# Optimization experiments

Measured on AMD Instinct MI355X. Metric: run time of the kernel, lower is better.

Reference implementation:

```python
import jax, jax.numpy as jnp
import numpy as np

N = 50000      # nodes
E = 1600000    # edges (before self loops)
B = 512        # graphs
D = 128        # gcn dim (constant across the 3 GAT layers)
H = 1024       # hidden_dim
O = 128        # output_dim
NEG_SLOPE = 0.2


def setup_inputs() -> dict:
    key = jax.random.key(0)
    ks = jax.random.split(key, 24)
    inp = {
        "x": jax.random.normal(ks[0], (N, D), jnp.float32),
        "edge_index": jax.random.randint(ks[1], (2, E), 0, N, dtype=jnp.int64),
        "edge_weight": jax.random.uniform(ks[2], (E,), jnp.float32),
        "batch": jnp.sort(jax.random.randint(ks[3], (N,), 0, B, dtype=jnp.int64)),
    }
    s = 1.0 / np.sqrt(D)
    for i in range(3):
        k = 4 + 4 * i
        inp[f"W{i+1}"] = jax.random.normal(ks[k], (D, D), jnp.float32) * s
        inp[f"as{i+1}"] = jax.random.normal(ks[k + 1], (D,), jnp.float32) * s
        inp[f"ad{i+1}"] = jax.random.normal(ks[k + 2], (D,), jnp.float32) * s
        inp[f"b{i+1}"] = jnp.zeros((D,), jnp.float32)
    inp["Wf1"] = jax.random.normal(ks[16], (D, H), jnp.float32) * s
    inp["bf1"] = jnp.zeros((H,), jnp.float32)
    inp["Wf2"] = jax.random.normal(ks[17], (H, O), jnp.float32) * (1.0 / np.sqrt(H))
    inp["bf2"] = jnp.zeros((O,), jnp.float32)
    return inp


def gat_conv(x, src, dst, W, a_src, a_dst, b):
    """PyG GATConv, heads=1: gather -> leakyrelu -> segment softmax -> scatter-add."""
    h = x @ W                                   # [N, D]
    e = jax.nn.leaky_relu(jnp.take(h @ a_src, src) + jnp.take(h @ a_dst, dst), NEG_SLOPE)  # [E']
    m = jax.ops.segment_max(e, dst, num_segments=N)
    ex = jnp.exp(e - m[dst])
    denom = jax.ops.segment_sum(ex, dst, num_segments=N)
    alpha = ex / denom[dst]                      # segment softmax over incoming edges
    out = jax.ops.segment_sum(alpha[:, None] * h[src], dst, num_segments=N)
    return out + b


def reference(x, edge_index, edge_weight, batch,
              W1, as1, ad1, b1, W2, as2, ad2, b2, W3, as3, ad3, b3,
              Wf1, bf1, Wf2, bf2):
    # GATConv adds self loops; edge_weight is unused by GATConv (faithful to original)
    loop = jnp.arange(N, dtype=edge_index.dtype)
    src = jnp.concatenate([edge_index[0], loop])
    dst = jnp.concatenate([edge_index[1], loop])

    h = gat_conv(x, src, dst, W1, as1, ad1, b1)
    h = jax.nn.relu(gat_conv(h, src, dst, W2, as2, ad2, b2))
    h = jax.nn.relu(gat_conv(h, src, dst, W3, as3, ad3, b3))

    # global mean pool (gep)
    sums = jax.ops.segment_sum(h, batch, num_segments=B)        # [B, D]
    counts = jax.ops.segment_sum(jnp.ones((N,), h.dtype), batch, num_segments=B)
    pooled = sums / jnp.maximum(counts, 1.0)[:, None]

    # MLP head; dropout is identity at inference
    o = jax.nn.relu(pooled) @ Wf1 + bf1
    o = jax.nn.relu(o) @ Wf2 + bf2
    return o
```

## Files before the change

### kernel.cpp

```cpp
#include <hip/hip_runtime.h>
#include <cstdint>
#include <cstddef>

#define NEG_SLOPE 0.2f

typedef _Float16 f16x8 __attribute__((ext_vector_type(8)));
typedef float f32x4v __attribute__((ext_vector_type(4)));

__device__ __forceinline__ unsigned enc_f(float f) {
  unsigned u = __float_as_uint(f);
  return (u & 0x80000000u) ? ~u : (u | 0x80000000u);
}
__device__ __forceinline__ float dec_f(unsigned u) {
  return (u & 0x80000000u) ? __uint_as_float(u ^ 0x80000000u) : __uint_as_float(~u);
}

#define AST 136
#define ABYTES (64 * AST * 2)
#define SMEM_BYTES (ABYTES + 4 * 64 * 2 * 4)

__global__ void k_bounds_prep(const int* __restrict__ batch, int N, int B,
                              int* __restrict__ gstart, unsigned* __restrict__ maxPart,
                              int* __restrict__ counts,
                              const float* __restrict__ W1, const float* __restrict__ W2,
                              const float* __restrict__ W3,
                              const float* __restrict__ Wf1, const float* __restrict__ Wf2,
                              _Float16* __restrict__ Wt1, _Float16* __restrict__ Wt2,
                              _Float16* __restrict__ Wt3,
                              _Float16* __restrict__ Wf1t, _Float16* __restrict__ Wf2t,
                              int nbb) {
  int b = blockIdx.x;
  if (b >= nbb) {
    int ti = b - nbb;
    const float* src;
    _Float16* dst;
    int lds_, ldd_, k0, n0;
    if (ti < 3) {
      src = (ti == 0) ? W1 : (ti == 1) ? W2 : W3;
      dst = (ti == 0) ? Wt1 : (ti == 1) ? Wt2 : Wt3;
      lds_ = 128; ldd_ = 128; k0 = 0; n0 = 0;
    } else if (ti < 11) {
      int j = ti - 3;
      src = Wf1; dst = Wf1t; lds_ = 1024; ldd_ = 128; k0 = 0; n0 = j * 128;
    } else {
      int j = ti - 11;
      src = Wf2; dst = Wf2t; lds_ = 128; ldd_ = 1024; k0 = j * 128; n0 = 0;
    }
    for (int i = threadIdx.x; i < 2048; i += 256) {
      int k = i >> 4, n8 = (i & 15) << 3;
      const float* s = &src[(size_t)(k0 + k) * lds_ + n0 + n8];
      float4 v0 = *(const float4*)&s[0];
      float4 v1 = *(const float4*)&s[4];
      dst[(size_t)(n0 + n8 + 0) * ldd_ + k0 + k] = (_Float16)v0.x;
      dst[(size_t)(n0 + n8 + 1) * ldd_ + k0 + k] = (_Float16)v0.y;
      dst[(size_t)(n0 + n8 + 2) * ldd_ + k0 + k] = (_Float16)v0.z;
      dst[(size_t)(n0 + n8 + 3) * ldd_ + k0 + k] = (_Float16)v0.w;
      dst[(size_t)(n0 + n8 + 4) * ldd_ + k0 + k] = (_Float16)v1.x;
      dst[(size_t)(n0 + n8 + 5) * ldd_ + k0 + k] = (_Float16)v1.y;
      dst[(size_t)(n0 + n8 + 6) * ldd_ + k0 + k] = (_Float16)v1.z;
      dst[(size_t)(n0 + n8 + 7) * ldd_ + k0 + k] = (_Float16)v1.w;
    }
    return;
  }
  int n = b * blockDim.x + threadIdx.x;
  if (n < 768) maxPart[n] = 0u;
  if (n >= N) return;
  counts[n] = 0;
  int cur = batch[n];
  if (n == 0) {
    for (int g = 0; g <= cur; g++) gstart[g] = 0;
  } else {
    int prev = batch[n - 1];
    for (int g = prev + 1; g <= cur; g++) gstart[g] = n;
  }
  if (n == N - 1) {
    for (int g = cur + 1; g <= B; g++) gstart[g] = N;
  }
}

__global__ void k_count_rank(const int* __restrict__ dst, int E,
                             int* counts, int* __restrict__ rank) {
  int e = blockIdx.x * blockDim.x + threadIdx.x;
  if (e < E) rank[e] = atomicAdd(&counts[dst[e]], 1);
}

__global__ __launch_bounds__(1024) void k_scan1(const int* __restrict__ counts, int N,
                                                int* __restrict__ row_ptr, int* __restrict__ part) {
  __shared__ int tmp[1024];
  int t = threadIdx.x;
  int i = blockIdx.x * 1024 + t;
  int v = (i < N) ? 1 + counts[i] : 0;
  tmp[t] = v;
  __syncthreads();
  for (int off = 1; off < 1024; off <<= 1) {
    int u = (t >= off) ? tmp[t - off] : 0;
    __syncthreads();
    tmp[t] += u;
    __syncthreads();
  }
  if (i < N) row_ptr[i + 1] = tmp[t];
  if (t == 1023) part[blockIdx.x] = tmp[t];
}

__global__ __launch_bounds__(1024) void k_scan3(int* __restrict__ row_ptr,
                                                const int* __restrict__ part, int N) {
  __shared__ int s_off;
  int bi = blockIdx.x;
  if (threadIdx.x == 0) {
    int run = 0;
    for (int b = 0; b < bi; b++) run += part[b];
    s_off = run;
    if (bi == 0) row_ptr[0] = 0;
  }
  __syncthreads();
  int i = bi * 1024 + threadIdx.x;
  if (i < N) row_ptr[i + 1] += s_off;
}

__device__ __forceinline__ void gemm_body(char* smem, int bx,
                                          const float* __restrict__ A32,
                                          const unsigned short* __restrict__ A16,
                                          const _Float16* __restrict__ WtG,
                                          unsigned short* __restrict__ hb,
                                          const float* __restrict__ asrc,
                                          const float* __restrict__ adst,
                                          float* __restrict__ sv, float* __restrict__ dv,
                                          unsigned* __restrict__ maxSlot, int M) {
  _Float16* Ah = (_Float16*)smem;
  float (*sred)[64][2] = (float (*)[64][2])(smem + ABYTES);
  int t = threadIdx.x;
  int rowbase = bx * 64;

  if (A16) {
    for (int i = t; i < 64 * 16; i += 256) {
      int r = i >> 4, c8 = (i & 15) << 3;
      int gr = rowbase + r;
      uint4 v = make_uint4(0u, 0u, 0u, 0u);
      if (gr < M) v = *(const uint4*)&A16[(size_t)gr * 128 + c8];
      *(uint4*)&Ah[r * AST + c8] = v;
    }
  } else {
    for (int i = t; i < 64 * 32; i += 256) {
      int r = i >> 5, c4 = (i & 31) << 2;
      int gr = rowbase + r;
      float4 v = make_float4(0.f, 0.f, 0.f, 0.f);
      if (gr < M) v = *(const float4*)&A32[(size_t)gr * 128 + c4];
      _Float16 tmp[4] = {(_Float16)v.x, (_Float16)v.y, (_Float16)v.z, (_Float16)v.w};
      *(short4*)&Ah[r * AST + c4] = *(short4*)tmp;
    }
  }
  __syncthreads();

  int wave = t >> 6, lane = t & 63, quad = lane >> 4, l15 = lane & 15;
  f32x4v acc[4][2];
#pragma unroll
  for (int mt = 0; mt < 4; mt++)
#pragma unroll
    for (int nt = 0; nt < 2; nt++) {
      acc[mt][nt][0] = 0.f; acc[mt][nt][1] = 0.f; acc[mt][nt][2] = 0.f; acc[mt][nt][3] = 0.f;
    }

#pragma unroll
  for (int s = 0; s < 4; s++) {
    int k0 = (s << 5) + (quad << 3);
    f16x8 af[4], bf[2];
#pragma unroll
    for (int mt = 0; mt < 4; mt++)
      af[mt] = *(f16x8*)&Ah[(mt * 16 + l15) * AST + k0];
#pragma unroll
    for (int nt = 0; nt < 2; nt++)
      bf[nt] = *(const f16x8*)&WtG[(size_t)(wave * 32 + nt * 16 + l15) * 128 + k0];
#pragma unroll
    for (int mt = 0; mt < 4; mt++)
#pragma unroll
      for (int nt = 0; nt < 2; nt++)
        acc[mt][nt] = __builtin_amdgcn_mfma_f32_16x16x32_f16(af[mt], bf[nt], acc[mt][nt], 0, 0, 0);
  }
  __syncthreads();

  float avv0 = asrc[wave * 32 + l15],      avv1 = asrc[wave * 32 + 16 + l15];
  float adv0 = adst[wave * 32 + l15],      adv1 = adst[wave * 32 + 16 + l15];
  _Float16* hS16 = (_Float16*)smem;
#pragma unroll
  for (int mt = 0; mt < 4; mt++) {
#pragma unroll
    for (int rr = 0; rr < 4; rr++) {
      int row = mt * 16 + quad * 4 + rr;
      hS16[row * AST + wave * 32 + l15]      = (_Float16)acc[mt][0][rr];
      hS16[row * AST + wave * 32 + 16 + l15] = (_Float16)acc[mt][1][rr];
      float ps = acc[mt][0][rr] * avv0 + acc[mt][1][rr] * avv1;
      float pd = acc[mt][0][rr] * adv0 + acc[mt][1][rr] * adv1;
#pragma unroll
      for (int mask = 8; mask; mask >>= 1) {
        ps += __shfl_xor(ps, mask);
        pd += __shfl_xor(pd, mask);
      }
      if (l15 == 0) { sred[wave][row][0] = ps; sred[wave][row][1] = pd; }
    }
  }
  __syncthreads();

  int tx = t & 31, ty = t >> 5;
#pragma unroll
  for (int r8 = 0; r8 < 8; r8++) {
    int row = r8 * 8 + ty;
    int gr = rowbase + row;
    if (gr < M)
      *(uint2*)&hb[(size_t)gr * 128 + tx * 4] = *(const uint2*)&hS16[row * AST + tx * 4];
  }

  if (t < 64) {
    int gr = rowbase + t;
    float ps = sred[0][t][0] + sred[1][t][0] + sred[2][t][0] + sred[3][t][0];
    float pd = sred[0][t][1] + sred[1][t][1] + sred[2][t][1] + sred[3][t][1];
    float wmax = -1e30f;
    if (gr < M) { sv[gr] = ps; dv[gr] = pd; wmax = ps; }
#pragma unroll
    for (int mask = 32; mask; mask >>= 1) wmax = fmaxf(wmax, __shfl_xor(wmax, mask));
    if (t == 0) atomicMax(&maxSlot[bx & 255], enc_f(wmax));
  }
}

__global__ __launch_bounds__(256) void k_fill_gemm(const int* __restrict__ src,
                                                   const int* __restrict__ dst,
                                                   const int* __restrict__ rank, int E, int N,
                                                   const int* __restrict__ row_ptr,
                                                   int* __restrict__ col,
                                                   const float* __restrict__ A32,
                                                   const _Float16* __restrict__ WtG,
                                                   unsigned short* __restrict__ hb,
                                                   const float* __restrict__ asrc,
                                                   const float* __restrict__ adst,
                                                   float* __restrict__ sv, float* __restrict__ dv,
                                                   unsigned* __restrict__ maxSlot, int Gg) {
  __shared__ __align__(16) char smem[SMEM_BYTES];
  int b = (int)blockIdx.x;
  bool isGemm = ((b % 9) == 4) && ((b / 9) < Gg);
  if (isGemm) {
    gemm_body(smem, b / 9, A32, (const unsigned short*)nullptr, WtG,
              hb, asrc, adst, sv, dv, maxSlot, N);
  } else {
    int nGemmBefore = (b >= 4) ? min((b - 4) / 9 + 1, Gg) : 0;
    int i = (b - nGemmBefore) * 256 + threadIdx.x;
    if (i < N) col[row_ptr[i]] = i;
    int e = i - N;
    if (e >= 0 && e < E) col[row_ptr[dst[e]] + 1 + rank[e]] = src[e];
  }
}

__global__ __launch_bounds__(256) void k_gemm_fused(const unsigned short* __restrict__ A16,
                                                    const _Float16* __restrict__ WtG,
                                                    unsigned short* __restrict__ hb,
                                                    const float* __restrict__ asrc,
                                                    const float* __restrict__ adst,
                                                    float* __restrict__ sv, float* __restrict__ dv,
                                                    unsigned* __restrict__ maxSlot, int M) {
  __shared__ __align__(16) char smem[SMEM_BYTES];
  gemm_body(smem, (int)blockIdx.x, (const float*)nullptr, A16, WtG,
            hb, asrc, adst, sv, dv, maxSlot, M);
}

__global__ __launch_bounds__(256) void k_agg(const unsigned short* __restrict__ hb,
                                             const float* __restrict__ sv,
                                             const float* __restrict__ dv,
                                             const int* __restrict__ row_ptr,
                                             const int* __restrict__ col,
                                             const float* __restrict__ bias,
                                             const unsigned* __restrict__ maxSlot,
                                             unsigned short* __restrict__ out16,
                                             int N, int relu) {
  int wid = (int)((blockIdx.x * (size_t)blockDim.x + threadIdx.x) >> 6);
  int lane = threadIdx.x & 63;
  if (wid >= N) return;

  unsigned mp = max(max(maxSlot[lane], maxSlot[lane + 64]),
                    max(maxSlot[lane + 128], maxSlot[lane + 192]));
#pragma unroll
  for (int off = 32; off; off >>= 1) mp = max(mp, __shfl_xor(mp, off));
  float maxS = dec_f(mp);

  int beg = row_ptr[wid], end = row_ptr[wid + 1];
  float dn = dv[wid];
  float m = maxS + dn;
  m = (m > 0.f) ? m : NEG_SLOPE * m;

  int g = lane >> 4, sub = lane & 15;
  const uint32_t* hbu = (const uint32_t*)hb;
  float acc[8];
#pragma unroll
  for (int k = 0; k < 8; k++) acc[k] = 0.f;
  float dsum = 0.f;

#define FETCH_SLOT(K, W, H)                                                \
  {                                                                        \
    int sl = ((K) << 2) + g;                                               \
    int sn = __shfl(sn_l, sl);                                             \
    W = __shfl(w_l, sl);                                                   \
    H = make_uint4(0u, 0u, 0u, 0u);                                        \
    if (sl < cnt) H = *(const uint4*)(hbu + (size_t)sn * 64 + sub * 4);    \
  }
#define ACC_SLOT(W, H)                                                     \
  {                                                                        \
    const _Float16* hp = (const _Float16*)&H;                              \
    _Pragma("unroll")                                                      \
    for (int q = 0; q < 8; q++) acc[q] += W * (float)hp[q];                \
  }

  for (int base = beg; base < end; base += 64) {
    int cnt = min(end - base, 64);

    int sn_l = 0;
    float w_l = 0.f;
    if (lane < cnt) {
      sn_l = col[base + lane];
      float e = sv[sn_l] + dn;
      e = (e > 0.f) ? e : NEG_SLOPE * e;
      w_l = __expf(e - m);
      dsum += w_l;
    }

    int kmaxW4 = (((cnt + 3) >> 2) + 3) & ~3;
    float wA, wB, wC, wD;
    uint4 hA, hB, hC, hD;
    FETCH_SLOT(0, wA, hA);
    FETCH_SLOT(1, wB, hB);
    FETCH_SLOT(2, wC, hC);
    FETCH_SLOT(3, wD, hD);
    for (int k = 4; k < kmaxW4; k += 4) {
      ACC_SLOT(wA, hA); FETCH_SLOT(k + 0, wA, hA);
      ACC_SLOT(wB, hB); FETCH_SLOT(k + 1, wB, hB);
      ACC_SLOT(wC, hC); FETCH_SLOT(k + 2, wC, hC);
      ACC_SLOT(wD, hD); FETCH_SLOT(k + 3, wD, hD);
    }
    ACC_SLOT(wA, hA);
    ACC_SLOT(wB, hB);
    ACC_SLOT(wC, hC);
    ACC_SLOT(wD, hD);
  }

#pragma unroll
  for (int off = 1; off < 64; off <<= 1) dsum += __shfl_xor(dsum, off);
#pragma unroll
  for (int k = 0; k < 8; k++) {
    acc[k] += __shfl_xor(acc[k], 16);
    acc[k] += __shfl_xor(acc[k], 32);
  }
  if (lane < 16) {
    float inv = 1.f / dsum;
    float o[8];
    const float* bp = &bias[sub * 8];
#pragma unroll
    for (int k = 0; k < 8; k++) {
      o[k] = acc[k] * inv + bp[k];
      if (relu) o[k] = fmaxf(o[k], 0.f);
    }
    _Float16 q[8];
#pragma unroll
    for (int k = 0; k < 8; k++) q[k] = (_Float16)o[k];
    *(uint4*)&out16[(size_t)wid * 128 + sub * 8] = *(uint4*)q;
  }
}

__global__ __launch_bounds__(256) void k_pool(const unsigned short* __restrict__ h16,
                                              const int* __restrict__ gstart,
                                              unsigned short* __restrict__ pooled16, int B) {
  __shared__ float red[4][128];
  int b = blockIdx.x, t = threadIdx.x;
  int c = t & 63, seg = t >> 6;
  int s0 = gstart[b], s1 = gstart[b + 1];
  int cnt = s1 - s0;
  int per = (cnt + 3) >> 2;
  int n0 = s0 + seg * per;
  int n1 = min(n0 + per, s1);
  const uint32_t* hu = (const uint32_t*)h16;
  float a0 = 0.f, a1 = 0.f;
  for (int n = n0; n < n1; n++) {
    union { uint32_t u; _Float16 h[2]; } cv;
    cv.u = hu[(size_t)n * 64 + c];
    a0 += (float)cv.h[0];
    a1 += (float)cv.h[1];
  }
  if (seg) { red[seg][2 * c] = a0; red[seg][2 * c + 1] = a1; }
  __syncthreads();
  if (seg == 0) {
    a0 += red[1][2 * c] + red[2][2 * c] + red[3][2 * c];
    a1 += red[1][2 * c + 1] + red[2][2 * c + 1] + red[3][2 * c + 1];
    float inv = 1.f / (float)(cnt > 0 ? cnt : 1);
    union { uint32_t u; _Float16 h[2]; } ov;
    ov.h[0] = (_Float16)fmaxf(a0 * inv, 0.f);
    ov.h[1] = (_Float16)fmaxf(a1 * inv, 0.f);
    *(uint32_t*)&pooled16[(size_t)b * 128 + 2 * c] = ov.u;
  }
}

__global__ __launch_bounds__(256) void k_mlp1(const unsigned short* __restrict__ P16,
                                              const _Float16* __restrict__ Wf1t,
                                              const float* __restrict__ bf1,
                                              unsigned short* __restrict__ H1g, int B, int nRow) {
  __shared__ __align__(16) _Float16 Ah[64 * AST];
  int bx = (int)blockIdx.x;
  int rowt = bx % nRow, colt = bx / nRow;
  int rowbase = rowt * 64;
  int t = threadIdx.x;

  for (int i = t; i < 64 * 16; i += 256) {
    int r = i >> 4, c8 = (i & 15) << 3;
    int gr = rowbase + r;
    uint4 v = make_uint4(0u, 0u, 0u, 0u);
    if (gr < B) v = *(const uint4*)&P16[(size_t)gr * 128 + c8];
    *(uint4*)&Ah[r * AST + c8] = v;
  }
  __syncthreads();

  int wave = t >> 6, lane = t & 63, quad = lane >> 4, l15 = lane & 15;
  int colbase = colt * 128 + wave * 32;
  f32x4v acc[4][2];
#pragma unroll
  for (int mt = 0; mt < 4; mt++)
#pragma unroll
    for (int nt = 0; nt < 2; nt++) {
      acc[mt][nt][0] = 0.f; acc[mt][nt][1] = 0.f; acc[mt][nt][2] = 0.f; acc[mt][nt][3] = 0.f;
    }
#pragma unroll
  for (int s = 0; s < 4; s++) {
    int k0 = (s << 5) + (quad << 3);
    f16x8 af[4], bf[2];
#pragma unroll
    for (int mt = 0; mt < 4; mt++)
      af[mt] = *(f16x8*)&Ah[(mt * 16 + l15) * AST + k0];
#pragma unroll
    for (int nt = 0; nt < 2; nt++)
      bf[nt] = *(const f16x8*)&Wf1t[(size_t)(colbase + nt * 16 + l15) * 128 + k0];
#pragma unroll
    for (int mt = 0; mt < 4; mt++)
#pragma unroll
      for (int nt = 0; nt < 2; nt++)
        acc[mt][nt] = __builtin_amdgcn_mfma_f32_16x16x32_f16(af[mt], bf[nt], acc[mt][nt], 0, 0, 0);
  }

  float b0 = bf1[colbase + l15], b1 = bf1[colbase + 16 + l15];
#pragma unroll
  for (int mt = 0; mt < 4; mt++)
#pragma unroll
    for (int rr = 0; rr < 4; rr++) {
      int gr = rowbase + mt * 16 + quad * 4 + rr;
      if (gr < B) {
        H1g[(size_t)gr * 1024 + colbase + l15] =
            (unsigned short)__builtin_bit_cast(unsigned short, (_Float16)fmaxf(acc[mt][0][rr] + b0, 0.f));
        H1g[(size_t)gr * 1024 + colbase + 16 + l15] =
            (unsigned short)__builtin_bit_cast(unsigned short, (_Float16)fmaxf(acc[mt][1][rr] + b1, 0.f));
      }
    }
}

__global__ __launch_bounds__(256) void k_mlp2(const unsigned short* __restrict__ H1g,
                                              const _Float16* __restrict__ Wf2t,
                                              const float* __restrict__ bf2,
                                              float* __restrict__ out, int B) {
  __shared__ __align__(16) _Float16 Ah[64 * AST];
  int rowbase = (int)blockIdx.x * 64;
  int t = threadIdx.x;
  int wave = t >> 6, lane = t & 63, quad = lane >> 4, l15 = lane & 15;

  f32x4v acc[4][2];
#pragma unroll
  for (int mt = 0; mt < 4; mt++)
#pragma unroll
    for (int nt = 0; nt < 2; nt++) {
      acc[mt][nt][0] = 0.f; acc[mt][nt][1] = 0.f; acc[mt][nt][2] = 0.f; acc[mt][nt][3] = 0.f;
    }

  for (int kc = 0; kc < 8; kc++) {
    for (int i = t; i < 64 * 16; i += 256) {
      int r = i >> 4, c8 = (i & 15) << 3;
      int gr = rowbase + r;
      uint4 v = make_uint4(0u, 0u, 0u, 0u);
      if (gr < B) v = *(const uint4*)&H1g[(size_t)gr * 1024 + kc * 128 + c8];
      *(uint4*)&Ah[r * AST + c8] = v;
    }
    __syncthreads();
#pragma unroll
    for (int s = 0; s < 4; s++) {
      int k0 = (s << 5) + (quad << 3);
      f16x8 af[4], bf[2];
#pragma unroll
      for (int mt = 0; mt < 4; mt++)
        af[mt] = *(f16x8*)&Ah[(mt * 16 + l15) * AST + k0];
#pragma unroll
      for (int nt = 0; nt < 2; nt++)
        bf[nt] = *(const f16x8*)&Wf2t[(size_t)(wave * 32 + nt * 16 + l15) * 1024 + kc * 128 + k0];
#pragma unroll
      for (int mt = 0; mt < 4; mt++)
#pragma unroll
        for (int nt = 0; nt < 2; nt++)
          acc[mt][nt] = __builtin_amdgcn_mfma_f32_16x16x32_f16(af[mt], bf[nt], acc[mt][nt], 0, 0, 0);
    }
    __syncthreads();
  }

  int col0 = wave * 32 + l15, col1 = col0 + 16;
  float b0 = bf2[col0], b1 = bf2[col1];
#pragma unroll
  for (int mt = 0; mt < 4; mt++)
#pragma unroll
    for (int rr = 0; rr < 4; rr++) {
      int gr = rowbase + mt * 16 + quad * 4 + rr;
      if (gr < B) {
        out[(size_t)gr * 128 + col0] = acc[mt][0][rr] + b0;
        out[(size_t)gr * 128 + col1] = acc[mt][1][rr] + b1;
      }
    }
}

extern "C" void kernel_launch(void* const* d_in, const int* in_sizes, int n_in,
                              void* d_out, int out_size, void* d_ws, size_t ws_size,
                              hipStream_t stream) {
  const float* x     = (const float*)d_in[0];
  const int*   ei    = (const int*)d_in[1];
  const int*   batch = (const int*)d_in[3];
  const float* W1 = (const float*)d_in[4];
  const float* as1 = (const float*)d_in[5];
  const float* ad1 = (const float*)d_in[6];
  const float* b1 = (const float*)d_in[7];
  const float* W2 = (const float*)d_in[8];
  const float* as2 = (const float*)d_in[9];
  const float* ad2 = (const float*)d_in[10];
  const float* b2 = (const float*)d_in[11];
  const float* W3 = (const float*)d_in[12];
  const float* as3 = (const float*)d_in[13];
  const float* ad3 = (const float*)d_in[14];
  const float* b3 = (const float*)d_in[15];
  const float* Wf1 = (const float*)d_in[16];
  const float* bf1 = (const float*)d_in[17];
  const float* Wf2 = (const float*)d_in[18];
  const float* bf2 = (const float*)d_in[19];

  const int N = in_sizes[0] / 128;
  const int E = in_sizes[1] / 2;
  const int B = out_size / 128;

  char* base_ws = (char*)d_ws;
  size_t off = 0;
  auto carve = [&](size_t bytes) -> void* {
    off = (off + 255) & ~(size_t)255;
    void* p = base_ws + off;
    off += bytes;
    return p;
  };
  int* counts   = (int*)carve((size_t)N * 4);
  int* row_ptr  = (int*)carve((size_t)(N + 1) * 4);
  int* rank     = (int*)carve((size_t)E * 4);
  int* col      = (int*)carve((size_t)(E + N) * 4);
  int* part     = (int*)carve(1024 * 4);
  int* gstart   = (int*)carve((size_t)(B + 1) * 4);
  unsigned* maxPart = (unsigned*)carve(768 * 4);
  float* sbuf   = (float*)carve((size_t)N * 4);
  float* dbuf   = (float*)carve((size_t)N * 4);
  unsigned short* hb  = (unsigned short*)carve((size_t)N * 128 * 2);
  unsigned short* a16 = (unsigned short*)carve((size_t)N * 128 * 2);
  unsigned short* pooled16 = (unsigned short*)carve((size_t)B * 128 * 2);
  unsigned short* H1g = (unsigned short*)carve((size_t)B * 1024 * 2);
  _Float16* Wt1 = (_Float16*)carve(128 * 128 * 2);
  _Float16* Wt2 = (_Float16*)carve(128 * 128 * 2);
  _Float16* Wt3 = (_Float16*)carve(128 * 128 * 2);
  _Float16* Wf1t = (_Float16*)carve((size_t)1024 * 128 * 2);
  _Float16* Wf2t = (_Float16*)carve((size_t)128 * 1024 * 2);

  const int* srcp = ei;
  const int* dstp = ei + E;
  const int nb = (N + 1023) / 1024;
  const int Gg = (N + 63) / 64;
  const int Gf = (E + N + 255) / 256;
  const int nbb = (N + 255) / 256;
  const int nRow = (B + 63) / 64;

  hipLaunchKernelGGL(k_bounds_prep, dim3(nbb + 19), dim3(256), 0, stream,
                     batch, N, B, gstart, maxPart, counts,
                     W1, W2, W3, Wf1, Wf2, Wt1, Wt2, Wt3, Wf1t, Wf2t, nbb);
  hipLaunchKernelGGL(k_count_rank, dim3((E + 255) / 256), dim3(256), 0, stream,
                     dstp, E, counts, rank);
  hipLaunchKernelGGL(k_scan1, dim3(nb), dim3(1024), 0, stream, counts, N, row_ptr, part);
  hipLaunchKernelGGL(k_scan3, dim3(nb), dim3(1024), 0, stream, row_ptr, part, N);

  hipLaunchKernelGGL(k_fill_gemm, dim3(Gf + Gg), dim3(256), 0, stream,
                     srcp, dstp, rank, E, N, row_ptr, col,
                     x, Wt1, hb, as1, ad1, sbuf, dbuf, maxPart + 0 * 256, Gg);

  hipLaunchKernelGGL(k_agg, dim3((N + 3) / 4), dim3(256), 0, stream,
                     hb, sbuf, dbuf, row_ptr, col, b1, maxPart + 0 * 256, a16, N, 0);

  hipLaunchKernelGGL(k_gemm_fused, dim3(Gg), dim3(256), 0, stream,
                     a16, Wt2, hb, as2, ad2, sbuf, dbuf, maxPart + 1 * 256, N);
  hipLaunchKernelGGL(k_agg, dim3((N + 3) / 4), dim3(256), 0, stream,
                     hb, sbuf, dbuf, row_ptr, col, b2, maxPart + 1 * 256, a16, N, 1);

  hipLaunchKernelGGL(k_gemm_fused, dim3(Gg), dim3(256), 0, stream,
                     a16, Wt3, hb, as3, ad3, sbuf, dbuf, maxPart + 2 * 256, N);
  hipLaunchKernelGGL(k_agg, dim3((N + 3) / 4), dim3(256), 0, stream,
                     hb, sbuf, dbuf, row_ptr, col, b3, maxPart + 2 * 256, a16, N, 1);

  hipLaunchKernelGGL(k_pool, dim3(B), dim3(256), 0, stream, a16, gstart, pooled16, B);
  hipLaunchKernelGGL(k_mlp1, dim3(nRow * 8), dim3(256), 0, stream,
                     pooled16, Wf1t, bf1, H1g, B, nRow);
  hipLaunchKernelGGL(k_mlp2, dim3(nRow), dim3(256), 0, stream,
                     H1g, Wf2t, bf2, (float*)d_out, B);
}
```

Before: 508.4 us.

## Merge edge counting into prep kernel and use 32-row GEMM tiles

Folds the per-edge atomic count/rank pass into the prep kernel as extra blocks, and zeroes the counts with a memset so the count blocks do not race with a reset inside the same launch. Layers 2 and 3 switch to a new GEMM kernel that handles 32 rows per block instead of 64. That doubles the grid for more parallelism and lower LDS use, and reads the B fragments straight from global memory. The aim is to cut one launch and raise occupancy. In exchange it re-reads the weights once per smaller tile and adds a memset call.

```diff
diff --git a/kernel.cpp b/kernel.cpp
--- a/kernel.cpp
+++ b/kernel.cpp
@@ -19,68 +19,67 @@
 #define ABYTES (64 * AST * 2)
 #define SMEM_BYTES (ABYTES + 4 * 64 * 2 * 4)
 
-__global__ void k_bounds_prep(const int* __restrict__ batch, int N, int B,
-                              int* __restrict__ gstart, unsigned* __restrict__ maxPart,
-                              int* __restrict__ counts,
-                              const float* __restrict__ W1, const float* __restrict__ W2,
-                              const float* __restrict__ W3,
-                              const float* __restrict__ Wf1, const float* __restrict__ Wf2,
-                              _Float16* __restrict__ Wt1, _Float16* __restrict__ Wt2,
-                              _Float16* __restrict__ Wt3,
-                              _Float16* __restrict__ Wf1t, _Float16* __restrict__ Wf2t,
-                              int nbb) {
+__global__ void k_count_prep(const int* __restrict__ dst, int E,
+                             int* counts, int* __restrict__ rank,
+                             const int* __restrict__ batch, int N, int B,
+                             int* __restrict__ gstart, unsigned* __restrict__ maxPart,
+                             const float* __restrict__ W1, const float* __restrict__ W2,
+                             const float* __restrict__ W3,
+                             const float* __restrict__ Wf1, const float* __restrict__ Wf2,
+                             _Float16* __restrict__ Wt1, _Float16* __restrict__ Wt2,
+                             _Float16* __restrict__ Wt3,
+                             _Float16* __restrict__ Wf1t, _Float16* __restrict__ Wf2t,
+                             int nbb) {
   int b = blockIdx.x;
-  if (b >= nbb) {
+  if (b < nbb) {
+    int n = b * blockDim.x + threadIdx.x;
+    if (n < 768) maxPart[n] = 0u;
+    if (n >= N) return;
+    int cur = batch[n];
+    if (n == 0) {
+      for (int g = 0; g <= cur; g++) gstart[g] = 0;
+    } else {
+      int prev = batch[n - 1];
+      for (int g = prev + 1; g <= cur; g++) gstart[g] = n;
+    }
+    if (n == N - 1) {
+      for (int g = cur + 1; g <= B; g++) gstart[g] = N;
+    }
+    return;
+  }
+  if (b < nbb + 19) {
     int ti = b - nbb;
     const float* src;
-    _Float16* dst;
+    _Float16* dstp_;
     int lds_, ldd_, k0, n0;
     if (ti < 3) {
       src = (ti == 0) ? W1 : (ti == 1) ? W2 : W3;
-      dst = (ti == 0) ? Wt1 : (ti == 1) ? Wt2 : Wt3;
+      dstp_ = (ti == 0) ? Wt1 : (ti == 1) ? Wt2 : Wt3;
       lds_ = 128; ldd_ = 128; k0 = 0; n0 = 0;
     } else if (ti < 11) {
       int j = ti - 3;
-      src = Wf1; dst = Wf1t; lds_ = 1024; ldd_ = 128; k0 = 0; n0 = j * 128;
+      src = Wf1; dstp_ = Wf1t; lds_ = 1024; ldd_ = 128; k0 = 0; n0 = j * 128;
     } else {
       int j = ti - 11;
-      src = Wf2; dst = Wf2t; lds_ = 128; ldd_ = 1024; k0 = j * 128; n0 = 0;
+      src = Wf2; dstp_ = Wf2t; lds_ = 128; ldd_ = 1024; k0 = j * 128; n0 = 0;
     }
     for (int i = threadIdx.x; i < 2048; i += 256) {
       int k = i >> 4, n8 = (i & 15) << 3;
       const float* s = &src[(size_t)(k0 + k) * lds_ + n0 + n8];
       float4 v0 = *(const float4*)&s[0];
       float4 v1 = *(const float4*)&s[4];
-      dst[(size_t)(n0 + n8 + 0) * ldd_ + k0 + k] = (_Float16)v0.x;
-      dst[(size_t)(n0 + n8 + 1) * ldd_ + k0 + k] = (_Float16)v0.y;
-      dst[(size_t)(n0 + n8 + 2) * ldd_ + k0 + k] = (_Float16)v0.z;
-      dst[(size_t)(n0 + n8 + 3) * ldd_ + k0 + k] = (_Float16)v0.w;
-      dst[(size_t)(n0 + n8 + 4) * ldd_ + k0 + k] = (_Float16)v1.x;
-      dst[(size_t)(n0 + n8 + 5) * ldd_ + k0 + k] = (_Float16)v1.y;
-      dst[(size_t)(n0 + n8 + 6) * ldd_ + k0 + k] = (_Float16)v1.z;
-      dst[(size_t)(n0 + n8 + 7) * ldd_ + k0 + k] = (_Float16)v1.w;
+      dstp_[(size_t)(n0 + n8 + 0) * ldd_ + k0 + k] = (_Float16)v0.x;
+      dstp_[(size_t)(n0 + n8 + 1) * ldd_ + k0 + k] = (_Float16)v0.y;
+      dstp_[(size_t)(n0 + n8 + 2) * ldd_ + k0 + k] = (_Float16)v0.z;
+      dstp_[(size_t)(n0 + n8 + 3) * ldd_ + k0 + k] = (_Float16)v0.w;
+      dstp_[(size_t)(n0 + n8 + 4) * ldd_ + k0 + k] = (_Float16)v1.x;
+      dstp_[(size_t)(n0 + n8 + 5) * ldd_ + k0 + k] = (_Float16)v1.y;
+      dstp_[(size_t)(n0 + n8 + 6) * ldd_ + k0 + k] = (_Float16)v1.z;
+      dstp_[(size_t)(n0 + n8 + 7) * ldd_ + k0 + k] = (_Float16)v1.w;
     }
     return;
   }
-  int n = b * blockDim.x + threadIdx.x;
-  if (n < 768) maxPart[n] = 0u;
-  if (n >= N) return;
-  counts[n] = 0;
-  int cur = batch[n];
-  if (n == 0) {
-    for (int g = 0; g <= cur; g++) gstart[g] = 0;
-  } else {
-    int prev = batch[n - 1];
-    for (int g = prev + 1; g <= cur; g++) gstart[g] = n;
-  }
-  if (n == N - 1) {
-    for (int g = cur + 1; g <= B; g++) gstart[g] = N;
-  }
-}
-
-__global__ void k_count_rank(const int* __restrict__ dst, int E,
-                             int* counts, int* __restrict__ rank) {
-  int e = blockIdx.x * blockDim.x + threadIdx.x;
+  int e = (b - nbb - 19) * 256 + threadIdx.x;
   if (e < E) rank[e] = atomicAdd(&counts[dst[e]], 1);
 }
 
@@ -248,16 +247,94 @@
   }
 }
 
-__global__ __launch_bounds__(256) void k_gemm_fused(const unsigned short* __restrict__ A16,
-                                                    const _Float16* __restrict__ WtG,
-                                                    unsigned short* __restrict__ hb,
-                                                    const float* __restrict__ asrc,
-                                                    const float* __restrict__ adst,
-                                                    float* __restrict__ sv, float* __restrict__ dv,
-                                                    unsigned* __restrict__ maxSlot, int M) {
-  __shared__ __align__(16) char smem[SMEM_BYTES];
-  gemm_body(smem, (int)blockIdx.x, (const float*)nullptr, A16, WtG,
-            hb, asrc, adst, sv, dv, maxSlot, M);
+__global__ __launch_bounds__(256) void k_gemm_fused32(const unsigned short* __restrict__ A16,
+                                                      const _Float16* __restrict__ WtG,
+                                                      unsigned short* __restrict__ hb,
+                                                      const float* __restrict__ asrc,
+                                                      const float* __restrict__ adst,
+                                                      float* __restrict__ sv, float* __restrict__ dv,
+                                                      unsigned* __restrict__ maxSlot, int M) {
+  __shared__ __align__(16) _Float16 Ah[32 * AST];
+  __shared__ float sred[4][32][2];
+  int t = threadIdx.x;
+  int rowbase = (int)blockIdx.x * 32;
+
+  for (int i = t; i < 32 * 16; i += 256) {
+    int r = i >> 4, c8 = (i & 15) << 3;
+    int gr = rowbase + r;
+    uint4 v = make_uint4(0u, 0u, 0u, 0u);
+    if (gr < M) v = *(const uint4*)&A16[(size_t)gr * 128 + c8];
+    *(uint4*)&Ah[r * AST + c8] = v;
+  }
+  __syncthreads();
+
+  int wave = t >> 6, lane = t & 63, quad = lane >> 4, l15 = lane & 15;
+  f32x4v acc[2][2];
+#pragma unroll
+  for (int mt = 0; mt < 2; mt++)
+#pragma unroll
+    for (int nt = 0; nt < 2; nt++) {
+      acc[mt][nt][0] = 0.f; acc[mt][nt][1] = 0.f; acc[mt][nt][2] = 0.f; acc[mt][nt][3] = 0.f;
+    }
+
+#pragma unroll
+  for (int s = 0; s < 4; s++) {
+    int k0 = (s << 5) + (quad << 3);
+    f16x8 af[2], bf[2];
+#pragma unroll
+    for (int mt = 0; mt < 2; mt++)
+      af[mt] = *(f16x8*)&Ah[(mt * 16 + l15) * AST + k0];
+#pragma unroll
+    for (int nt = 0; nt < 2; nt++)
+      bf[nt] = *(const f16x8*)&WtG[(size_t)(wave * 32 + nt * 16 + l15) * 128 + k0];
+#pragma unroll
+    for (int mt = 0; mt < 2; mt++)
+#pragma unroll
+      for (int nt = 0; nt < 2; nt++)
+        acc[mt][nt] = __builtin_amdgcn_mfma_f32_16x16x32_f16(af[mt], bf[nt], acc[mt][nt], 0, 0, 0);
+  }
+  __syncthreads();
+
+  float avv0 = asrc[wave * 32 + l15],      avv1 = asrc[wave * 32 + 16 + l15];
+  float adv0 = adst[wave * 32 + l15],      adv1 = adst[wave * 32 + 16 + l15];
+#pragma unroll
+  for (int mt = 0; mt < 2; mt++) {
+#pragma unroll
+    for (int rr = 0; rr < 4; rr++) {
+      int row = mt * 16 + quad * 4 + rr;
+      Ah[row * AST + wave * 32 + l15]      = (_Float16)acc[mt][0][rr];
+      Ah[row * AST + wave * 32 + 16 + l15] = (_Float16)acc[mt][1][rr];
+      float ps = acc[mt][0][rr] * avv0 + acc[mt][1][rr] * avv1;
+      float pd = acc[mt][0][rr] * adv0 + acc[mt][1][rr] * adv1;
+#pragma unroll
+      for (int mask = 8; mask; mask >>= 1) {
+        ps += __shfl_xor(ps, mask);
+        pd += __shfl_xor(pd, mask);
+      }
+      if (l15 == 0) { sred[wave][row][0] = ps; sred[wave][row][1] = pd; }
+    }
+  }
+  __syncthreads();
+
+  int tx = t & 31, ty = t >> 5;
+#pragma unroll
+  for (int r4 = 0; r4 < 4; r4++) {
+    int row = r4 * 8 + ty;
+    int gr = rowbase + row;
+    if (gr < M)
+      *(uint2*)&hb[(size_t)gr * 128 + tx * 4] = *(const uint2*)&Ah[row * AST + tx * 4];
+  }
+
+  if (t < 32) {
+    int gr = rowbase + t;
+    float ps = sred[0][t][0] + sred[1][t][0] + sred[2][t][0] + sred[3][t][0];
+    float pd = sred[0][t][1] + sred[1][t][1] + sred[2][t][1] + sred[3][t][1];
+    float wmax = -1e30f;
+    if (gr < M) { sv[gr] = ps; dv[gr] = pd; wmax = ps; }
+#pragma unroll
+    for (int mask = 16; mask; mask >>= 1) wmax = fmaxf(wmax, __shfl_xor(wmax, mask));
+    if (t == 0) atomicMax(&maxSlot[blockIdx.x & 255], enc_f(wmax));
+  }
 }
 
 __global__ __launch_bounds__(256) void k_agg(const unsigned short* __restrict__ hb,
@@ -570,15 +647,17 @@
   const int* dstp = ei + E;
   const int nb = (N + 1023) / 1024;
   const int Gg = (N + 63) / 64;
+  const int Gg2 = (N + 31) / 32;
   const int Gf = (E + N + 255) / 256;
   const int nbb = (N + 255) / 256;
+  const int Cb = (E + 255) / 256;
   const int nRow = (B + 63) / 64;
 
-  hipLaunchKernelGGL(k_bounds_prep, dim3(nbb + 19), dim3(256), 0, stream,
-                     batch, N, B, gstart, maxPart, counts,
+  hipMemsetAsync(counts, 0, (size_t)N * 4, stream);
+  hipLaunchKernelGGL(k_count_prep, dim3(nbb + 19 + Cb), dim3(256), 0, stream,
+                     dstp, E, counts, rank,
+                     batch, N, B, gstart, maxPart,
                      W1, W2, W3, Wf1, Wf2, Wt1, Wt2, Wt3, Wf1t, Wf2t, nbb);
-  hipLaunchKernelGGL(k_count_rank, dim3((E + 255) / 256), dim3(256), 0, stream,
-                     dstp, E, counts, rank);
   hipLaunchKernelGGL(k_scan1, dim3(nb), dim3(1024), 0, stream, counts, N, row_ptr, part);
   hipLaunchKernelGGL(k_scan3, dim3(nb), dim3(1024), 0, stream, row_ptr, part, N);
 
@@ -589,12 +668,12 @@
   hipLaunchKernelGGL(k_agg, dim3((N + 3) / 4), dim3(256), 0, stream,
                      hb, sbuf, dbuf, row_ptr, col, b1, maxPart + 0 * 256, a16, N, 0);
 
-  hipLaunchKernelGGL(k_gemm_fused, dim3(Gg), dim3(256), 0, stream,
+  hipLaunchKernelGGL(k_gemm_fused32, dim3(Gg2), dim3(256), 0, stream,
                      a16, Wt2, hb, as2, ad2, sbuf, dbuf, maxPart + 1 * 256, N);
   hipLaunchKernelGGL(k_agg, dim3((N + 3) / 4), dim3(256), 0, stream,
                      hb, sbuf, dbuf, row_ptr, col, b2, maxPart + 1 * 256, a16, N, 1);
 
-  hipLaunchKernelGGL(k_gemm_fused, dim3(Gg), dim3(256), 0, stream,
+  hipLaunchKernelGGL(k_gemm_fused32, dim3(Gg2), dim3(256), 0, stream,
                      a16, Wt3, hb, as3, ad3, sbuf, dbuf, maxPart + 2 * 256, N);
   hipLaunchKernelGGL(k_agg, dim3((N + 3) / 4), dim3(256), 0, stream,
                      hb, sbuf, dbuf, row_ptr, col, b3, maxPart + 2 * 256, a16, N, 1);
```

New measurement: 499.8 us, median of 2. About the same (-1.7%).

## Overlap next-layer GEMM with second-half aggregation using double-buffered features

Applied to the files above, without the earlier changes.

Each GAT aggregation pass is split into two node halves. The first half is aggregated alone. The second half's aggregation blocks are interleaved in one launch with GEMM blocks that transform the already-finished first half for the next layer, and a trailing GEMM launch covers the remaining rows. This needs ping-pong buffers for hb, sv and dv. The count/rank kernel is also merged into the prep kernel, with counts zeroed by a memset, to save a launch. The intent is to hide GEMM time behind the memory-bound gather, at the cost of more launches and extra workspace.

```diff
diff --git a/kernel.cpp b/kernel.cpp
--- a/kernel.cpp
+++ b/kernel.cpp
@@ -19,68 +19,67 @@
 #define ABYTES (64 * AST * 2)
 #define SMEM_BYTES (ABYTES + 4 * 64 * 2 * 4)
 
-__global__ void k_bounds_prep(const int* __restrict__ batch, int N, int B,
-                              int* __restrict__ gstart, unsigned* __restrict__ maxPart,
-                              int* __restrict__ counts,
-                              const float* __restrict__ W1, const float* __restrict__ W2,
-                              const float* __restrict__ W3,
-                              const float* __restrict__ Wf1, const float* __restrict__ Wf2,
-                              _Float16* __restrict__ Wt1, _Float16* __restrict__ Wt2,
-                              _Float16* __restrict__ Wt3,
-                              _Float16* __restrict__ Wf1t, _Float16* __restrict__ Wf2t,
-                              int nbb) {
+__global__ void k_count_prep(const int* __restrict__ dst, int E,
+                             int* counts, int* __restrict__ rank,
+                             const int* __restrict__ batch, int N, int B,
+                             int* __restrict__ gstart, unsigned* __restrict__ maxPart,
+                             const float* __restrict__ W1, const float* __restrict__ W2,
+                             const float* __restrict__ W3,
+                             const float* __restrict__ Wf1, const float* __restrict__ Wf2,
+                             _Float16* __restrict__ Wt1, _Float16* __restrict__ Wt2,
+                             _Float16* __restrict__ Wt3,
+                             _Float16* __restrict__ Wf1t, _Float16* __restrict__ Wf2t,
+                             int nbb) {
   int b = blockIdx.x;
-  if (b >= nbb) {
+  if (b < nbb) {
+    int n = b * blockDim.x + threadIdx.x;
+    if (n < 768) maxPart[n] = 0u;
+    if (n >= N) return;
+    int cur = batch[n];
+    if (n == 0) {
+      for (int g = 0; g <= cur; g++) gstart[g] = 0;
+    } else {
+      int prev = batch[n - 1];
+      for (int g = prev + 1; g <= cur; g++) gstart[g] = n;
+    }
+    if (n == N - 1) {
+      for (int g = cur + 1; g <= B; g++) gstart[g] = N;
+    }
+    return;
+  }
+  if (b < nbb + 19) {
     int ti = b - nbb;
     const float* src;
-    _Float16* dst;
+    _Float16* dstp_;
     int lds_, ldd_, k0, n0;
     if (ti < 3) {
       src = (ti == 0) ? W1 : (ti == 1) ? W2 : W3;
-      dst = (ti == 0) ? Wt1 : (ti == 1) ? Wt2 : Wt3;
+      dstp_ = (ti == 0) ? Wt1 : (ti == 1) ? Wt2 : Wt3;
       lds_ = 128; ldd_ = 128; k0 = 0; n0 = 0;
     } else if (ti < 11) {
       int j = ti - 3;
-      src = Wf1; dst = Wf1t; lds_ = 1024; ldd_ = 128; k0 = 0; n0 = j * 128;
+      src = Wf1; dstp_ = Wf1t; lds_ = 1024; ldd_ = 128; k0 = 0; n0 = j * 128;
     } else {
       int j = ti - 11;
-      src = Wf2; dst = Wf2t; lds_ = 128; ldd_ = 1024; k0 = j * 128; n0 = 0;
+      src = Wf2; dstp_ = Wf2t; lds_ = 128; ldd_ = 1024; k0 = j * 128; n0 = 0;
     }
     for (int i = threadIdx.x; i < 2048; i += 256) {
       int k = i >> 4, n8 = (i & 15) << 3;
       const float* s = &src[(size_t)(k0 + k) * lds_ + n0 + n8];
       float4 v0 = *(const float4*)&s[0];
       float4 v1 = *(const float4*)&s[4];
-      dst[(size_t)(n0 + n8 + 0) * ldd_ + k0 + k] = (_Float16)v0.x;
-      dst[(size_t)(n0 + n8 + 1) * ldd_ + k0 + k] = (_Float16)v0.y;
-      dst[(size_t)(n0 + n8 + 2) * ldd_ + k0 + k] = (_Float16)v0.z;
-      dst[(size_t)(n0 + n8 + 3) * ldd_ + k0 + k] = (_Float16)v0.w;
-      dst[(size_t)(n0 + n8 + 4) * ldd_ + k0 + k] = (_Float16)v1.x;
-      dst[(size_t)(n0 + n8 + 5) * ldd_ + k0 + k] = (_Float16)v1.y;
-      dst[(size_t)(n0 + n8 + 6) * ldd_ + k0 + k] = (_Float16)v1.z;
-      dst[(size_t)(n0 + n8 + 7) * ldd_ + k0 + k] = (_Float16)v1.w;
+      dstp_[(size_t)(n0 + n8 + 0) * ldd_ + k0 + k] = (_Float16)v0.x;
+      dstp_[(size_t)(n0 + n8 + 1) * ldd_ + k0 + k] = (_Float16)v0.y;
+      dstp_[(size_t)(n0 + n8 + 2) * ldd_ + k0 + k] = (_Float16)v0.z;
+      dstp_[(size_t)(n0 + n8 + 3) * ldd_ + k0 + k] = (_Float16)v0.w;
+      dstp_[(size_t)(n0 + n8 + 4) * ldd_ + k0 + k] = (_Float16)v1.x;
+      dstp_[(size_t)(n0 + n8 + 5) * ldd_ + k0 + k] = (_Float16)v1.y;
+      dstp_[(size_t)(n0 + n8 + 6) * ldd_ + k0 + k] = (_Float16)v1.z;
+      dstp_[(size_t)(n0 + n8 + 7) * ldd_ + k0 + k] = (_Float16)v1.w;
     }
     return;
   }
-  int n = b * blockDim.x + threadIdx.x;
-  if (n < 768) maxPart[n] = 0u;
-  if (n >= N) return;
-  counts[n] = 0;
-  int cur = batch[n];
-  if (n == 0) {
-    for (int g = 0; g <= cur; g++) gstart[g] = 0;
-  } else {
-    int prev = batch[n - 1];
-    for (int g = prev + 1; g <= cur; g++) gstart[g] = n;
-  }
-  if (n == N - 1) {
-    for (int g = cur + 1; g <= B; g++) gstart[g] = N;
-  }
-}
-
-__global__ void k_count_rank(const int* __restrict__ dst, int E,
-                             int* counts, int* __restrict__ rank) {
-  int e = blockIdx.x * blockDim.x + threadIdx.x;
+  int e = (b - nbb - 19) * 256 + threadIdx.x;
   if (e < E) rank[e] = atomicAdd(&counts[dst[e]], 1);
 }
 
@@ -218,6 +217,150 @@
 #pragma unroll
     for (int mask = 32; mask; mask >>= 1) wmax = fmaxf(wmax, __shfl_xor(wmax, mask));
     if (t == 0) atomicMax(&maxSlot[bx & 255], enc_f(wmax));
+  }
+}
+
+__device__ __forceinline__ void agg_body(int aggBlk,
+                                         const unsigned short* __restrict__ hb,
+                                         const float* __restrict__ sv,
+                                         const float* __restrict__ dv,
+                                         const int* __restrict__ row_ptr,
+                                         const int* __restrict__ col,
+                                         const float* __restrict__ bias,
+                                         const unsigned* __restrict__ maxSlot,
+                                         unsigned short* __restrict__ out16,
+                                         int n0, int n1, int relu) {
+  int wid = n0 + aggBlk * 4 + (threadIdx.x >> 6);
+  int lane = threadIdx.x & 63;
+  if (wid >= n1) return;
+
+  unsigned mp = max(max(maxSlot[lane], maxSlot[lane + 64]),
+                    max(maxSlot[lane + 128], maxSlot[lane + 192]));
+#pragma unroll
+  for (int off = 32; off; off >>= 1) mp = max(mp, __shfl_xor(mp, off));
+  float maxS = dec_f(mp);
+
+  int beg = row_ptr[wid], end = row_ptr[wid + 1];
+  float dn = dv[wid];
+  float m = maxS + dn;
+  m = (m > 0.f) ? m : NEG_SLOPE * m;
+
+  int g = lane >> 4, sub = lane & 15;
+  const uint32_t* hbu = (const uint32_t*)hb;
+  float acc[8];
+#pragma unroll
+  for (int k = 0; k < 8; k++) acc[k] = 0.f;
+  float dsum = 0.f;
+
+#define FETCH_SLOT(K, W, H)                                                \
+  {                                                                        \
+    int sl = ((K) << 2) + g;                                               \
+    int sn = __shfl(sn_l, sl);                                             \
+    W = __shfl(w_l, sl);                                                   \
+    H = make_uint4(0u, 0u, 0u, 0u);                                        \
+    if (sl < cnt) H = *(const uint4*)(hbu + (size_t)sn * 64 + sub * 4);    \
+  }
+#define ACC_SLOT(W, H)                                                     \
+  {                                                                        \
+    const _Float16* hp = (const _Float16*)&H;                              \
+    _Pragma("unroll")                                                      \
+    for (int q = 0; q < 8; q++) acc[q] += W * (float)hp[q];                \
+  }
+
+  for (int base = beg; base < end; base += 64) {
+    int cnt = min(end - base, 64);
+
+    int sn_l = 0;
+    float w_l = 0.f;
+    if (lane < cnt) {
+      sn_l = col[base + lane];
+      float e = sv[sn_l] + dn;
+      e = (e > 0.f) ? e : NEG_SLOPE * e;
+      w_l = __expf(e - m);
+      dsum += w_l;
+    }
+
+    int kmaxW4 = (((cnt + 3) >> 2) + 3) & ~3;
+    float wA, wB, wC, wD;
+    uint4 hA, hB, hC, hD;
+    FETCH_SLOT(0, wA, hA);
+    FETCH_SLOT(1, wB, hB);
+    FETCH_SLOT(2, wC, hC);
+    FETCH_SLOT(3, wD, hD);
+    for (int k = 4; k < kmaxW4; k += 4) {
+      ACC_SLOT(wA, hA); FETCH_SLOT(k + 0, wA, hA);
+      ACC_SLOT(wB, hB); FETCH_SLOT(k + 1, wB, hB);
+      ACC_SLOT(wC, hC); FETCH_SLOT(k + 2, wC, hC);
+      ACC_SLOT(wD, hD); FETCH_SLOT(k + 3, wD, hD);
+    }
+    ACC_SLOT(wA, hA);
+    ACC_SLOT(wB, hB);
+    ACC_SLOT(wC, hC);
+    ACC_SLOT(wD, hD);
+  }
+
+#pragma unroll
+  for (int off = 1; off < 64; off <<= 1) dsum += __shfl_xor(dsum, off);
+#pragma unroll
+  for (int k = 0; k < 8; k++) {
+    acc[k] += __shfl_xor(acc[k], 16);
+    acc[k] += __shfl_xor(acc[k], 32);
+  }
+  if (lane < 16) {
+    float inv = 1.f / dsum;
+    float o[8];
+    const float* bp = &bias[sub * 8];
+#pragma unroll
+    for (int k = 0; k < 8; k++) {
+      o[k] = acc[k] * inv + bp[k];
+      if (relu) o[k] = fmaxf(o[k], 0.f);
+    }
+    _Float16 q[8];
+#pragma unroll
+    for (int k = 0; k < 8; k++) q[k] = (_Float16)o[k];
+    *(uint4*)&out16[(size_t)wid * 128 + sub * 8] = *(uint4*)q;
+  }
+}
+
+__global__ __launch_bounds__(256) void k_agg(const unsigned short* __restrict__ hb,
+                                             const float* __restrict__ sv,
+                                             const float* __restrict__ dv,
+                                             const int* __restrict__ row_ptr,
+                                             const int* __restrict__ col,
+                                             const float* __restrict__ bias,
+                                             const unsigned* __restrict__ maxSlot,
+                                             unsigned short* __restrict__ out16,
+                                             int n0, int n1, int relu) {
+  agg_body((int)blockIdx.x, hb, sv, dv, row_ptr, col, bias, maxSlot, out16, n0, n1, relu);
+}
+
+__global__ __launch_bounds__(256) void k_agg_gemm(const unsigned short* __restrict__ hb_r,
+                                                  const float* __restrict__ sv_r,
+                                                  const float* __restrict__ dv_r,
+                                                  const int* __restrict__ row_ptr,
+                                                  const int* __restrict__ col,
+                                                  const float* __restrict__ bias,
+                                                  const unsigned* __restrict__ maxSlot_r,
+                                                  unsigned short* __restrict__ a16,
+                                                  int n0, int n1, int relu,
+                                                  const _Float16* __restrict__ WtG,
+                                                  unsigned short* __restrict__ hb_w,
+                                                  const float* __restrict__ asrc,
+                                                  const float* __restrict__ adst,
+                                                  float* __restrict__ sv_w,
+                                                  float* __restrict__ dv_w,
+                                                  unsigned* __restrict__ maxSlot_w,
+                                                  int Gh1, int R, int N) {
+  __shared__ __align__(16) char smem[SMEM_BYTES];
+  int b = (int)blockIdx.x;
+  int half = R >> 1;
+  bool isGemm = ((b % R) == half) && ((b / R) < Gh1);
+  if (isGemm) {
+    gemm_body(smem, b / R, (const float*)nullptr, a16, WtG,
+              hb_w, asrc, adst, sv_w, dv_w, maxSlot_w, N);
+  } else {
+    int nGB = (b >= half) ? min((b - half) / R + 1, Gh1) : 0;
+    agg_body(b - nGB, hb_r, sv_r, dv_r, row_ptr, col, bias, maxSlot_r, a16, n0, n1, relu);
   }
 }
 
@@ -248,117 +391,16 @@
   }
 }
 
-__global__ __launch_bounds__(256) void k_gemm_fused(const unsigned short* __restrict__ A16,
+__global__ __launch_bounds__(256) void k_gemm_range(const unsigned short* __restrict__ A16,
                                                     const _Float16* __restrict__ WtG,
                                                     unsigned short* __restrict__ hb,
                                                     const float* __restrict__ asrc,
                                                     const float* __restrict__ adst,
                                                     float* __restrict__ sv, float* __restrict__ dv,
-                                                    unsigned* __restrict__ maxSlot, int M) {
+                                                    unsigned* __restrict__ maxSlot, int M, int bxOff) {
   __shared__ __align__(16) char smem[SMEM_BYTES];
-  gemm_body(smem, (int)blockIdx.x, (const float*)nullptr, A16, WtG,
+  gemm_body(smem, bxOff + (int)blockIdx.x, (const float*)nullptr, A16, WtG,
             hb, asrc, adst, sv, dv, maxSlot, M);
-}
-
-__global__ __launch_bounds__(256) void k_agg(const unsigned short* __restrict__ hb,
-                                             const float* __restrict__ sv,
-                                             const float* __restrict__ dv,
-                                             const int* __restrict__ row_ptr,
-                                             const int* __restrict__ col,
-                                             const float* __restrict__ bias,
-                                             const unsigned* __restrict__ maxSlot,
-                                             unsigned short* __restrict__ out16,
-                                             int N, int relu) {
-  int wid = (int)((blockIdx.x * (size_t)blockDim.x + threadIdx.x) >> 6);
-  int lane = threadIdx.x & 63;
-  if (wid >= N) return;
-
-  unsigned mp = max(max(maxSlot[lane], maxSlot[lane + 64]),
-                    max(maxSlot[lane + 128], maxSlot[lane + 192]));
-#pragma unroll
-  for (int off = 32; off; off >>= 1) mp = max(mp, __shfl_xor(mp, off));
-  float maxS = dec_f(mp);
-
-  int beg = row_ptr[wid], end = row_ptr[wid + 1];
-  float dn = dv[wid];
-  float m = maxS + dn;
-  m = (m > 0.f) ? m : NEG_SLOPE * m;
-
-  int g = lane >> 4, sub = lane & 15;
-  const uint32_t* hbu = (const uint32_t*)hb;
-  float acc[8];
-#pragma unroll
-  for (int k = 0; k < 8; k++) acc[k] = 0.f;
-  float dsum = 0.f;
-
-#define FETCH_SLOT(K, W, H)                                                \
-  {                                                                        \
-    int sl = ((K) << 2) + g;                                               \
-    int sn = __shfl(sn_l, sl);                                             \
-    W = __shfl(w_l, sl);                                                   \
-    H = make_uint4(0u, 0u, 0u, 0u);                                        \
-    if (sl < cnt) H = *(const uint4*)(hbu + (size_t)sn * 64 + sub * 4);    \
-  }
-#define ACC_SLOT(W, H)                                                     \
-  {                                                                        \
-    const _Float16* hp = (const _Float16*)&H;                              \
-    _Pragma("unroll")                                                      \
-    for (int q = 0; q < 8; q++) acc[q] += W * (float)hp[q];                \
-  }
-
-  for (int base = beg; base < end; base += 64) {
-    int cnt = min(end - base, 64);
-
-    int sn_l = 0;
-    float w_l = 0.f;
-    if (lane < cnt) {
-      sn_l = col[base + lane];
-      float e = sv[sn_l] + dn;
-      e = (e > 0.f) ? e : NEG_SLOPE * e;
-      w_l = __expf(e - m);
-      dsum += w_l;
-    }
-
-    int kmaxW4 = (((cnt + 3) >> 2) + 3) & ~3;
-    float wA, wB, wC, wD;
-    uint4 hA, hB, hC, hD;
-    FETCH_SLOT(0, wA, hA);
-    FETCH_SLOT(1, wB, hB);
-    FETCH_SLOT(2, wC, hC);
-    FETCH_SLOT(3, wD, hD);
-    for (int k = 4; k < kmaxW4; k += 4) {
-      ACC_SLOT(wA, hA); FETCH_SLOT(k + 0, wA, hA);
-      ACC_SLOT(wB, hB); FETCH_SLOT(k + 1, wB, hB);
-      ACC_SLOT(wC, hC); FETCH_SLOT(k + 2, wC, hC);
-      ACC_SLOT(wD, hD); FETCH_SLOT(k + 3, wD, hD);
-    }
-    ACC_SLOT(wA, hA);
-    ACC_SLOT(wB, hB);
-    ACC_SLOT(wC, hC);
-    ACC_SLOT(wD, hD);
-  }
-
-#pragma unroll
-  for (int off = 1; off < 64; off <<= 1) dsum += __shfl_xor(dsum, off);
-#pragma unroll
-  for (int k = 0; k < 8; k++) {
-    acc[k] += __shfl_xor(acc[k], 16);
-    acc[k] += __shfl_xor(acc[k], 32);
-  }
-  if (lane < 16) {
-    float inv = 1.f / dsum;
-    float o[8];
-    const float* bp = &bias[sub * 8];
-#pragma unroll
-    for (int k = 0; k < 8; k++) {
-      o[k] = acc[k] * inv + bp[k];
-      if (relu) o[k] = fmaxf(o[k], 0.f);
-    }
-    _Float16 q[8];
-#pragma unroll
-    for (int k = 0; k < 8; k++) q[k] = (_Float16)o[k];
-    *(uint4*)&out16[(size_t)wid * 128 + sub * 8] = *(uint4*)q;
-  }
 }
 
 __global__ __launch_bounds__(256) void k_pool(const unsigned short* __restrict__ h16,
@@ -554,9 +596,12 @@
   int* part     = (int*)carve(1024 * 4);
   int* gstart   = (int*)carve((size_t)(B + 1) * 4);
   unsigned* maxPart = (unsigned*)carve(768 * 4);
-  float* sbuf   = (float*)carve((size_t)N * 4);
-  float* dbuf   = (float*)carve((size_t)N * 4);
-  unsigned short* hb  = (unsigned short*)carve((size_t)N * 128 * 2);
+  float* svA    = (float*)carve((size_t)N * 4);
+  float* dvA    = (float*)carve((size_t)N * 4);
+  float* svB    = (float*)carve((size_t)N * 4);
+  float* dvB    = (float*)carve((size_t)N * 4);
+  unsigned short* hbA = (unsigned short*)carve((size_t)N * 128 * 2);
+  unsigned short* hbB = (unsigned short*)carve((size_t)N * 128 * 2);
   unsigned short* a16 = (unsigned short*)carve((size_t)N * 128 * 2);
   unsigned short* pooled16 = (unsigned short*)carve((size_t)B * 128 * 2);
   unsigned short* H1g = (unsigned short*)carve((size_t)B * 1024 * 2);
@@ -572,32 +617,47 @@
   const int Gg = (N + 63) / 64;
   const int Gf = (E + N + 255) / 256;
   const int nbb = (N + 255) / 256;
+  const int Cb = (E + 255) / 256;
   const int nRow = (B + 63) / 64;
 
-  hipLaunchKernelGGL(k_bounds_prep, dim3(nbb + 19), dim3(256), 0, stream,
-                     batch, N, B, gstart, maxPart, counts,
+  int Nh = ((N / 2 + 63) / 64) * 64;
+  if (Nh >= N) Nh = (N > 64) ? ((N - 64) / 64) * 64 : 0;
+  const int Gh1 = Nh / 64;
+  const int Ah1 = (Nh + 3) / 4;
+  const int Ah2 = (N - Nh + 3) / 4;
+  int R = (Gh1 > 0) ? (Ah2 + Gh1) / Gh1 : 2;
+  if (R < 2) R = 2;
+
+  hipMemsetAsync(counts, 0, (size_t)N * 4, stream);
+  hipLaunchKernelGGL(k_count_prep, dim3(nbb + 19 + Cb), dim3(256), 0, stream,
+                     dstp, E, counts, rank,
+                     batch, N, B, gstart, maxPart,
                      W1, W2, W3, Wf1, Wf2, Wt1, Wt2, Wt3, Wf1t, Wf2t, nbb);
-  hipLaunchKernelGGL(k_count_rank, dim3((E + 255) / 256), dim3(256), 0, stream,
-                     dstp, E, counts, rank);
   hipLaunchKernelGGL(k_scan1, dim3(nb), dim3(1024), 0, stream, counts, N, row_ptr, part);
   hipLaunchKernelGGL(k_scan3, dim3(nb), dim3(1024), 0, stream, row_ptr, part, N);
 
   hipLaunchKernelGGL(k_fill_gemm, dim3(Gf + Gg), dim3(256), 0, stream,
                      srcp, dstp, rank, E, N, row_ptr, col,
-                     x, Wt1, hb, as1, ad1, sbuf, dbuf, maxPart + 0 * 256, Gg);
+                     x, Wt1, hbA, as1, ad1, svA, dvA, maxPart + 0 * 256, Gg);
+
+  hipLaunchKernelGGL(k_agg, dim3(Ah1), dim3(256), 0, stream,
+                     hbA, svA, dvA, row_ptr, col, b1, maxPart + 0 * 256, a16, 0, Nh, 0);
+  hipLaunchKernelGGL(k_agg_gemm, dim3(Ah2 + Gh1), dim3(256), 0, stream,
+                     hbA, svA, dvA, row_ptr, col, b1, maxPart + 0 * 256, a16, Nh, N, 0,
+                     Wt2, hbB, as2, ad2, svB, dvB, maxPart + 1 * 256, Gh1, R, N);
+  hipLaunchKernelGGL(k_gemm_range, dim3(Gg - Gh1), dim3(256), 0, stream,
+                     a16, Wt2, hbB, as2, ad2, svB, dvB, maxPart + 1 * 256, N, Gh1);
+
+  hipLaunchKernelGGL(k_agg, dim3(Ah1), dim3(256), 0, stream,
+                     hbB, svB, dvB, row_ptr, col, b2, maxPart + 1 * 256, a16, 0, Nh, 1);
+  hipLaunchKernelGGL(k_agg_gemm, dim3(Ah2 + Gh1), dim3(256), 0, stream,
+                     hbB, svB, dvB, row_ptr, col, b2, maxPart + 1 * 256, a16, Nh, N, 1,
+                     Wt3, hbA, as3, ad3, svA, dvA, maxPart + 2 * 256, Gh1, R, N);
+  hipLaunchKernelGGL(k_gemm_range, dim3(Gg - Gh1), dim3(256), 0, stream,
+                     a16, Wt3, hbA, as3, ad3, svA, dvA, maxPart + 2 * 256, N, Gh1);
 
   hipLaunchKernelGGL(k_agg, dim3((N + 3) / 4), dim3(256), 0, stream,
-                     hb, sbuf, dbuf, row_ptr, col, b1, maxPart + 0 * 256, a16, N, 0);
-
-  hipLaunchKernelGGL(k_gemm_fused, dim3(Gg), dim3(256), 0, stream,
-                     a16, Wt2, hb, as2, ad2, sbuf, dbuf, maxPart + 1 * 256, N);
-  hipLaunchKernelGGL(k_agg, dim3((N + 3) / 4), dim3(256), 0, stream,
-                     hb, sbuf, dbuf, row_ptr, col, b2, maxPart + 1 * 256, a16, N, 1);
-
-  hipLaunchKernelGGL(k_gemm_fused, dim3(Gg), dim3(256), 0, stream,
-                     a16, Wt3, hb, as3, ad3, sbuf, dbuf, maxPart + 2 * 256, N);
-  hipLaunchKernelGGL(k_agg, dim3((N + 3) / 4), dim3(256), 0, stream,
-                     hb, sbuf, dbuf, row_ptr, col, b3, maxPart + 2 * 256, a16, N, 1);
+                     hbA, svA, dvA, row_ptr, col, b3, maxPart + 2 * 256, a16, 0, N, 1);
 
   hipLaunchKernelGGL(k_pool, dim3(B), dim3(256), 0, stream, a16, gstart, pooled16, B);
   hipLaunchKernelGGL(k_mlp1, dim3(nRow * 8), dim3(256), 0, stream,
```

Measured after the change: 564.1 us. +11.0%, slower.
